# Optimization experiments

Hardware: AMD Instinct MI355X
Metric: run time of the kernel (lower is better)

## Reference

```python
import jax, jax.numpy as jnp
import numpy as np
from jax import lax

EOS_TOKEN = 2
VOCAB = 32000
EMB = 256
HID = 512
BATCH = 64
SEQ = 1024
N_EOS = 32  # EOS tokens per sequence (fixed so output shape is deterministic)


def setup_inputs() -> dict:
    key = jax.random.key(0)
    k_tok, k_pos, k_emb, k_wi, k_wh, k_bi, k_bh = jax.random.split(key, 7)
    # tokens in [3, VOCAB) so EOS only appears where we place it
    tokens = jax.random.randint(k_tok, (BATCH, SEQ), 3, VOCAB)
    # place exactly N_EOS EOS tokens per row at sorted random positions
    perms = jax.vmap(lambda k: jax.random.permutation(k, SEQ))(
        jax.random.split(k_pos, BATCH))
    eos_pos = jnp.sort(perms[:, :N_EOS], axis=1)  # [B, N_EOS]
    rows = jnp.arange(BATCH)[:, None]
    tokens = tokens.at[rows, eos_pos].set(EOS_TOKEN)
    s = 1.0 / np.sqrt(HID)
    return {
        "input_tokens": tokens.astype(jnp.int64) if jax.config.jax_enable_x64 else tokens.astype(jnp.int32),
        "emb_table": jax.random.normal(k_emb, (VOCAB, EMB), jnp.float32),
        "w_ih": jax.random.uniform(k_wi, (3 * HID, EMB), jnp.float32, -s, s),
        "w_hh": jax.random.uniform(k_wh, (3 * HID, HID), jnp.float32, -s, s),
        "b_ih": jax.random.uniform(k_bi, (3 * HID,), jnp.float32, -s, s),
        "b_hh": jax.random.uniform(k_bh, (3 * HID,), jnp.float32, -s, s),
    }


def _gru(embedded, w_ih, w_hh, b_ih, b_hh):
    # embedded: [S, B, E]; PyTorch GRU cell math, h0 = 0
    S, B, _ = embedded.shape
    H = w_hh.shape[1]
    # precompute input projections for all timesteps: [S, B, 3H]
    gi_all = jnp.einsum('sbe,ge->sbg', embedded, w_ih) + b_ih

    def step(h, gi):
        gh = h @ w_hh.T + b_hh                      # [B, 3H]
        i_r, i_z, i_n = jnp.split(gi, 3, axis=-1)
        h_r, h_z, h_n = jnp.split(gh, 3, axis=-1)
        r = jax.nn.sigmoid(i_r + h_r)
        z = jax.nn.sigmoid(i_z + h_z)
        n = jnp.tanh(i_n + r * h_n)
        h_new = (1.0 - z) * n + z * h
        return h_new, h_new

    h0 = jnp.zeros((B, H), embedded.dtype)
    _, outs = lax.scan(step, h0, gi_all)           # outs: [S, B, H]
    return outs


def reference(input_tokens, emb_table, w_ih, w_hh, b_ih, b_hh):
    tokens_t = input_tokens.T                       # [S, B]
    embedded = emb_table[tokens_t]                  # [S, B, E]
    outputs = _gru(embedded, w_ih, w_hh, b_ih, b_hh)  # [S, B, H]

    mask = tokens_t == EOS_TOKEN                    # [S, B]
    counts = mask.sum(0)
    C = int(np.max(np.asarray(counts)))             # deterministic = N_EOS by construction
    # compaction: k-th EOS output of column b goes to c[k, b]
    dest = jnp.where(mask, jnp.cumsum(mask, axis=0) - 1, C)  # [S, B]; C = dump row
    B, H = outputs.shape[1], outputs.shape[2]
    c = jnp.zeros((C + 1, B, H), outputs.dtype)
    c = c.at[dest, jnp.arange(B)[None, :]].add(jnp.where(mask[..., None], outputs, 0.0))
    return c[:C]
```

## Files before the change

kernel.cpp:

```cpp
#include <hip/hip_runtime.h>
#include <hip/hip_bf16.h>

typedef __attribute__((ext_vector_type(8))) short  bf16x8;
typedef __attribute__((ext_vector_type(4))) float  f32x4;
typedef __attribute__((ext_vector_type(4))) unsigned int u32x4;

#define EOS 2
#define S 1024
#define B 64
#define E 256
#define H 512
#define SENT 0xFFFFFFFFu

#define HBUF_OFF 4096
#define SLOT (2 * B * H)
#define DEST_OFF (HBUF_OFF + 4 * SLOT * 2)

#define AT_ST(p, v) __hip_atomic_store((p), (v), __ATOMIC_RELAXED, __HIP_MEMORY_SCOPE_AGENT)

__device__ __forceinline__ unsigned short f2bf(float f) {
    unsigned int u = __builtin_bit_cast(unsigned int, f);
    unsigned int r = (u + 0x7FFFu + ((u >> 16) & 1u)) >> 16;
    return (unsigned short)r;
}
__device__ __forceinline__ float bf2f(unsigned short s) {
    unsigned int u = ((unsigned int)s) << 16;
    return __builtin_bit_cast(float, u);
}
__device__ __forceinline__ unsigned int pk2(float x, float y) {
    unsigned int ux = __builtin_bit_cast(unsigned int, x) + 0x8000u;
    unsigned int uy = __builtin_bit_cast(unsigned int, y) + 0x8000u;
    return (ux >> 16) | (uy & 0xFFFF0000u);
}
__device__ __forceinline__ bf16x8 pack8hu(float4 a, float4 b) {
    union { unsigned int d[4]; bf16x8 v; } u;
    u.d[0] = pk2(a.x, a.y); u.d[1] = pk2(a.z, a.w);
    u.d[2] = pk2(b.x, b.y); u.d[3] = pk2(b.z, b.w);
    return u.v;
}
__device__ __forceinline__ bf16x8 pack8rne(float4 a, float4 b) {
    union { unsigned short s[8]; bf16x8 v; } u;
    u.s[0] = f2bf(a.x); u.s[1] = f2bf(a.y); u.s[2] = f2bf(a.z); u.s[3] = f2bf(a.w);
    u.s[4] = f2bf(b.x); u.s[5] = f2bf(b.y); u.s[6] = f2bf(b.z); u.s[7] = f2bf(b.w);
    return u.v;
}

__global__ __launch_bounds__(256) void dest_kernel(const int* __restrict__ tokens,
                                                   signed char* __restrict__ dest8) {
    const int b = blockIdx.x, tid = threadIdx.x;
    const int l = tid & 63, w = tid >> 6;
    const int base = tid * 4;
    int m[4], cnt = 0;
#pragma unroll
    for (int i = 0; i < 4; ++i) {
        int tok = tokens[b * S + base + i];
        m[i] = (tok == EOS) ? 1 : 0;
        cnt += m[i];
    }
    int inc = cnt;
#pragma unroll
    for (int d = 1; d < 64; d <<= 1) {
        int v = __shfl_up(inc, d, 64);
        if (l >= d) inc += v;
    }
    __shared__ int wt[4];
    if (l == 63) wt[w] = inc;
    __syncthreads();
    int off = 0;
    for (int k = 0; k < 4; ++k)
        if (k < w) off += wt[k];
    int run = off + inc - cnt;
#pragma unroll
    for (int i = 0; i < 4; ++i) {
        dest8[(base + i) * B + b] = m[i] ? (signed char)run : (signed char)-1;
        run += m[i];
    }
}

__global__ __launch_bounds__(256, 1) void gru_kernel(
    const int* __restrict__ tokens, const float* __restrict__ emb,
    const float* __restrict__ w_ih, const float* __restrict__ w_hh,
    const float* __restrict__ b_ih, const float* __restrict__ b_hh,
    const signed char* __restrict__ dest8,
    char* ws, float* __restrict__ out) {

    const int tid = threadIdx.x;
    const int wv = tid >> 6;
    const int l = tid & 63;
    const int l15 = l & 15, quad = l >> 4;
    const int blk = blockIdx.x;
    const int w = blk & 3;
    const int j4 = blk >> 2;
    const int unit = (j4 * 4 + wv) * 16 + l15;
    const int koff = quad * 8;
    const int brow = w * 16 + l15;

    unsigned short* hbuf = (unsigned short*)(ws + HBUF_OFF);

    __shared__ alignas(16) unsigned short sh[2][16][512];

    bf16x8 Wh[3][16];
#pragma unroll
    for (int g = 0; g < 3; ++g)
#pragma unroll
        for (int kt = 0; kt < 16; ++kt) {
            const float* p = &w_hh[(size_t)(g * H + unit) * H + kt * 32 + koff];
            Wh[g][kt] = pack8rne(*(const float4*)p, *(const float4*)(p + 4));
        }
    bf16x8 Wi[3][8];
#pragma unroll
    for (int g = 0; g < 3; ++g)
#pragma unroll
        for (int kt = 0; kt < 8; ++kt) {
            const float* p = &w_ih[(size_t)(g * H + unit) * E + kt * 32 + koff];
            Wi[g][kt] = pack8rne(*(const float4*)p, *(const float4*)(p + 4));
        }
    const float bi0 = b_ih[unit], bi1 = b_ih[H + unit], bi2 = b_ih[2 * H + unit];
    const float bh0 = b_hh[unit], bh1 = b_hh[H + unit], bh2 = b_hh[2 * H + unit];

    float hown[4] = {0.f, 0.f, 0.f, 0.f};
    int tok_next = tokens[brow * S];
    int budget = 1 << 21;

    const int p_st  = tid >> 7;
    const int rr_st = (tid >> 3) & 15;
    const int t7    = tid & 7;

    for (int t = 0; t < S; ++t) {
        const int tok = tok_next;
        const float* er = &emb[(size_t)tok * E + koff];
        float4 ef[8][2];
#pragma unroll
        for (int kt = 0; kt < 8; ++kt) {
            ef[kt][0] = *(const float4*)(er + kt * 32);
            ef[kt][1] = *(const float4*)(er + kt * 32 + 4);
        }
        if (t + 1 < S) tok_next = tokens[brow * S + t + 1];
        unsigned int dword =
            *(const unsigned int*)&dest8[t * B + w * 16 + quad * 4];

        f32x4 gi0 = {bi0, bi0, bi0, bi0};
        f32x4 gi1 = {bi1, bi1, bi1, bi1};
        f32x4 gi2 = {bi2, bi2, bi2, bi2};
#pragma unroll
        for (int kt = 0; kt < 8; ++kt) {
            bf16x8 af = pack8hu(ef[kt][0], ef[kt][1]);
            gi0 = __builtin_amdgcn_mfma_f32_16x16x32_bf16(af, Wi[0][kt], gi0, 0, 0, 0);
            gi1 = __builtin_amdgcn_mfma_f32_16x16x32_bf16(af, Wi[1][kt], gi1, 0, 0, 0);
            gi2 = __builtin_amdgcn_mfma_f32_16x16x32_bf16(af, Wi[2][kt], gi2, 0, 0, 0);
        }

        {
            const unsigned short* hs = hbuf + (size_t)(t & 3) * SLOT;
            const unsigned short* gp =
                hs + (size_t)p_st * (B * H) + (size_t)(w * 16 + rr_st) * H + t7 * 8;
            u32x4 gr[8];
            unsigned int bad;
            do {
                asm volatile(
                    "global_load_dwordx4 %0, %8, off sc1\n\t"
                    "global_load_dwordx4 %1, %8, off offset:128 sc1\n\t"
                    "global_load_dwordx4 %2, %8, off offset:256 sc1\n\t"
                    "global_load_dwordx4 %3, %8, off offset:384 sc1\n\t"
                    "global_load_dwordx4 %4, %8, off offset:512 sc1\n\t"
                    "global_load_dwordx4 %5, %8, off offset:640 sc1\n\t"
                    "global_load_dwordx4 %6, %8, off offset:768 sc1\n\t"
                    "global_load_dwordx4 %7, %8, off offset:896 sc1\n\t"
                    "s_waitcnt vmcnt(0)"
                    : "=&v"(gr[0]), "=&v"(gr[1]), "=&v"(gr[2]), "=&v"(gr[3]),
                      "=&v"(gr[4]), "=&v"(gr[5]), "=&v"(gr[6]), "=&v"(gr[7])
                    : "v"(gp)
                    : "memory");
                bad = 0;
#pragma unroll
                for (int c = 0; c < 8; ++c)
                    bad |= (unsigned)((gr[c][0] == SENT) | (gr[c][1] == SENT) |
                                      (gr[c][2] == SENT) | (gr[c][3] == SENT));
            } while (bad && --budget > 0);
#pragma unroll
            for (int c = 0; c < 8; ++c) {
                int pos = ((t7 + 8 * c) ^ (rr_st & 7)) * 8;
                *(u32x4*)&sh[p_st][rr_st][pos] = gr[c];
            }
        }

        {
            unsigned short* rs = hbuf + (size_t)((t + 2) & 3) * SLOT;
            const size_t rbase = (size_t)(w * 16 + (tid >> 4)) * H + j4 * 64;
            unsigned int* ph = (unsigned int*)(rs + rbase) + (tid & 15) * 2;
            unsigned int* pl = (unsigned int*)(rs + B * H + rbase) + (tid & 15) * 2;
            AT_ST(ph, SENT); AT_ST(ph + 1, SENT);
            AT_ST(pl, SENT); AT_ST(pl + 1, SENT);
        }
        __syncthreads();

        f32x4 a0 = {bh0, bh0, bh0, bh0};
        f32x4 a1 = {bh1, bh1, bh1, bh1};
        f32x4 a2 = {bh2, bh2, bh2, bh2};
#pragma unroll
        for (int kt = 0; kt < 16; ++kt) {
            const int pos = ((kt * 4 + quad) ^ (l15 & 7)) * 8;
            bf16x8 ah = *(const bf16x8*)&sh[0][l15][pos];
            bf16x8 al = *(const bf16x8*)&sh[1][l15][pos];
            a0 = __builtin_amdgcn_mfma_f32_16x16x32_bf16(ah, Wh[0][kt], a0, 0, 0, 0);
            a1 = __builtin_amdgcn_mfma_f32_16x16x32_bf16(ah, Wh[1][kt], a1, 0, 0, 0);
            a2 = __builtin_amdgcn_mfma_f32_16x16x32_bf16(ah, Wh[2][kt], a2, 0, 0, 0);
            a0 = __builtin_amdgcn_mfma_f32_16x16x32_bf16(al, Wh[0][kt], a0, 0, 0, 0);
            a1 = __builtin_amdgcn_mfma_f32_16x16x32_bf16(al, Wh[1][kt], a1, 0, 0, 0);
            a2 = __builtin_amdgcn_mfma_f32_16x16x32_bf16(al, Wh[2][kt], a2, 0, 0, 0);
        }

        float hval[4];
        unsigned int pkv[4];
#pragma unroll
        for (int r = 0; r < 4; ++r) {
            float rg = 1.f / (1.f + __expf(-(gi0[r] + a0[r])));
            float zg = 1.f / (1.f + __expf(-(gi1[r] + a1[r])));
            float x = gi2[r] + rg * a2[r];
            x = fminf(15.f, fmaxf(-15.f, x));
            float e = __expf(-2.f * x);
            float ng = (1.f - e) / (1.f + e);
            float h = (1.f - zg) * ng + zg * hown[r];
            hown[r] = h; hval[r] = h;
            unsigned short hi16 = f2bf(h);
            unsigned short lo16 = f2bf(h - bf2f(hi16));
            pkv[r] = ((unsigned int)lo16 << 16) | (unsigned int)hi16;
        }

        asm volatile("s_waitcnt vmcnt(0)" ::: "memory");
        {
            unsigned short* hd = hbuf + (size_t)((t + 1) & 3) * SLOT;
            unsigned int* hd_hi32 = (unsigned int*)hd;
            unsigned int* hd_lo32 = (unsigned int*)(hd + B * H);
            const bool even = (l15 & 1) == 0;
#pragma unroll
            for (int r = 0; r < 4; ++r) {
                const int b = w * 16 + quad * 4 + r;
                unsigned int sw = (unsigned int)__shfl_xor((int)pkv[r], 1);
                unsigned int val = even ? ((pkv[r] & 0xFFFFu) | (sw << 16))
                                        : ((sw >> 16) | (pkv[r] & 0xFFFF0000u));
                unsigned int didx = ((unsigned int)(b * H + unit)) >> 1;
                AT_ST((even ? hd_hi32 : hd_lo32) + didx, val);
            }
        }
        __syncthreads();

#pragma unroll
        for (int r = 0; r < 4; ++r) {
            const int b = w * 16 + quad * 4 + r;
            int db = (int)(signed char)((dword >> (8 * r)) & 0xFFu);
            if (db >= 0)
                out[((size_t)(db * B + b)) * H + unit] = hval[r];
        }
    }
}

extern "C" void kernel_launch(void* const* d_in, const int* in_sizes, int n_in,
                              void* d_out, int out_size, void* d_ws, size_t ws_size,
                              hipStream_t stream) {
    const int*   tokens = (const int*)d_in[0];
    const float* emb    = (const float*)d_in[1];
    const float* w_ih   = (const float*)d_in[2];
    const float* w_hh   = (const float*)d_in[3];
    const float* b_ih   = (const float*)d_in[4];
    const float* b_hh   = (const float*)d_in[5];
    float* out = (float*)d_out;

    char* ws = (char*)d_ws;
    signed char* dest8 = (signed char*)(ws + DEST_OFF);

    hipMemsetAsync(ws + HBUF_OFF, 0, SLOT * 2, stream);
    hipMemsetAsync(ws + HBUF_OFF + SLOT * 2, 0xFF, 3 * SLOT * 2, stream);
    dest_kernel<<<B, 256, 0, stream>>>(tokens, dest8);
    gru_kernel<<<32, 256, 0, stream>>>(tokens, emb, w_ih, w_hh, b_ih, b_hh,
                                       dest8, ws, out);
}
```

Before: 5.376 ms.

## Pin all recurrence blocks to one XCC and relax h-exchange coherence scope

Launches 256 blocks and uses a per-XCC atomic ticket so the first XCC to gather 32 blocks does the work and the other blocks exit. With every worker on one XCC sharing an L2, the hidden-state exchange switches from agent-scope stores and sc1 loads to workgroup-scope stores and sc0 loads. This is meant to cut the per-timestep cross-block synchronisation latency. It risks stale data, since coherence now depends on L2 sharing, and it can fail if no XCC ever collects 32 co-resident blocks.

```diff
diff --git a/kernel.cpp b/kernel.cpp
--- a/kernel.cpp
+++ b/kernel.cpp
@@ -16,7 +16,7 @@
 #define SLOT (2 * B * H)
 #define DEST_OFF (HBUF_OFF + 4 * SLOT * 2)
 
-#define AT_ST(p, v) __hip_atomic_store((p), (v), __ATOMIC_RELAXED, __HIP_MEMORY_SCOPE_AGENT)
+#define AT_ST(p, v) __hip_atomic_store((p), (v), __ATOMIC_RELAXED, __HIP_MEMORY_SCOPE_WORKGROUP)
 
 __device__ __forceinline__ unsigned short f2bf(float f) {
     unsigned int u = __builtin_bit_cast(unsigned int, f);
@@ -84,11 +84,46 @@
     const signed char* __restrict__ dest8,
     char* ws, float* __restrict__ out) {
 
+    __shared__ int s_slot;
+    if (threadIdx.x == 0) {
+        unsigned int xcc;
+        asm volatile("s_getreg_b32 %0, hwreg(HW_REG_XCC_ID)" : "=s"(xcc));
+        xcc &= 7u;
+        int* cnt = (int*)ws;
+        int* win = (int*)(ws + 32);
+        int ticket = __hip_atomic_fetch_add(&cnt[xcc], 1, __ATOMIC_RELAXED,
+                                            __HIP_MEMORY_SCOPE_AGENT);
+        int slot = -1;
+        if (ticket < 32) {
+            if (ticket == 31) {
+                int exp = -1;
+                __hip_atomic_compare_exchange_strong(win, &exp, (int)xcc,
+                    __ATOMIC_RELAXED, __ATOMIC_RELAXED, __HIP_MEMORY_SCOPE_AGENT);
+            }
+            int wv = -1, bud = 1 << 18;
+            do {
+                wv = __hip_atomic_load(win, __ATOMIC_RELAXED,
+                                       __HIP_MEMORY_SCOPE_AGENT);
+            } while (wv == -1 && --bud > 0);
+            if (wv == -1) {
+                int exp = -1;
+                __hip_atomic_compare_exchange_strong(win, &exp, (int)xcc,
+                    __ATOMIC_RELAXED, __ATOMIC_RELAXED, __HIP_MEMORY_SCOPE_AGENT);
+                wv = __hip_atomic_load(win, __ATOMIC_RELAXED,
+                                       __HIP_MEMORY_SCOPE_AGENT);
+            }
+            if (wv == (int)xcc) slot = ticket;
+        }
+        s_slot = slot;
+    }
+    __syncthreads();
+    const int blk = s_slot;
+    if (blk < 0) return;
+
     const int tid = threadIdx.x;
     const int wv = tid >> 6;
     const int l = tid & 63;
     const int l15 = l & 15, quad = l >> 4;
-    const int blk = blockIdx.x;
     const int w = blk & 3;
     const int j4 = blk >> 2;
     const int unit = (j4 * 4 + wv) * 16 + l15;
@@ -158,14 +193,14 @@
             unsigned int bad;
             do {
                 asm volatile(
-                    "global_load_dwordx4 %0, %8, off sc1\n\t"
-                    "global_load_dwordx4 %1, %8, off offset:128 sc1\n\t"
-                    "global_load_dwordx4 %2, %8, off offset:256 sc1\n\t"
-                    "global_load_dwordx4 %3, %8, off offset:384 sc1\n\t"
-                    "global_load_dwordx4 %4, %8, off offset:512 sc1\n\t"
-                    "global_load_dwordx4 %5, %8, off offset:640 sc1\n\t"
-                    "global_load_dwordx4 %6, %8, off offset:768 sc1\n\t"
-                    "global_load_dwordx4 %7, %8, off offset:896 sc1\n\t"
+                    "global_load_dwordx4 %0, %8, off sc0\n\t"
+                    "global_load_dwordx4 %1, %8, off offset:128 sc0\n\t"
+                    "global_load_dwordx4 %2, %8, off offset:256 sc0\n\t"
+                    "global_load_dwordx4 %3, %8, off offset:384 sc0\n\t"
+                    "global_load_dwordx4 %4, %8, off offset:512 sc0\n\t"
+                    "global_load_dwordx4 %5, %8, off offset:640 sc0\n\t"
+                    "global_load_dwordx4 %6, %8, off offset:768 sc0\n\t"
+                    "global_load_dwordx4 %7, %8, off offset:896 sc0\n\t"
                     "s_waitcnt vmcnt(0)"
                     : "=&v"(gr[0]), "=&v"(gr[1]), "=&v"(gr[2]), "=&v"(gr[3]),
                       "=&v"(gr[4]), "=&v"(gr[5]), "=&v"(gr[6]), "=&v"(gr[7])
@@ -269,9 +304,11 @@
     char* ws = (char*)d_ws;
     signed char* dest8 = (signed char*)(ws + DEST_OFF);
 
+    hipMemsetAsync(ws, 0, 32, stream);
+    hipMemsetAsync(ws + 32, 0xFF, 4, stream);
     hipMemsetAsync(ws + HBUF_OFF, 0, SLOT * 2, stream);
     hipMemsetAsync(ws + HBUF_OFF + SLOT * 2, 0xFF, 3 * SLOT * 2, stream);
     dest_kernel<<<B, 256, 0, stream>>>(tokens, dest8);
-    gru_kernel<<<32, 256, 0, stream>>>(tokens, emb, w_ih, w_hh, b_ih, b_hh,
-                                       dest8, ws, out);
-}
+    gru_kernel<<<256, 256, 0, stream>>>(tokens, emb, w_ih, w_hh, b_ih, b_hh,
+                                        dest8, ws, out);
+}
```

Measured after the change: 5.115 ms (median of 3 runs). 4.9% less time.
